# Performance work log

Hardware: AMD Instinct MI355X
Metric: run time of the kernel (lower is better)

The kernel has to match this reference:

```python
import jax, jax.numpy as jnp
from jax import lax
import numpy as np

ARG_NAMES = ('x w1 b1 bn1_g bn1_b bn1_m bn1_v w2 b2 bn2_g bn2_b bn2_m bn2_v w3 b3 w4 b4 '
             'attn_w attn_b attn_u g0_w1 g0_b1 g0_w2 g0_b2 g1_w1 g1_b1 g1_w2 g1_b2 '
             'g2_w1 g2_b1 g2_w2 g2_b2 c_w1 c_b1 c_w2 c_b2 c_w3 c_b3 c_w4 c_b4').split()


def _conv1d(x, w, b, stride, pad):
    # x: [N, C, L], w: [O, I, K]
    y = lax.conv_general_dilated(x, w, (stride,), [(pad, pad)],
                                 dimension_numbers=('NCH', 'OIH', 'NCH'))
    return y + b[None, :, None]


def _bn(x, g, b, m, v, eps=1e-5):
    # eval-mode BatchNorm1d over channel dim of [N, C, L]
    inv = g / jnp.sqrt(v + eps)
    return (x - m[None, :, None]) * inv[None, :, None] + b[None, :, None]


def _forward(x, w1, b1, bn1_g, bn1_b, bn1_m, bn1_v, w2, b2, bn2_g, bn2_b, bn2_m, bn2_v,
             w3, b3, w4, b4, attn_w, attn_b, attn_u,
             g0_w1, g0_b1, g0_w2, g0_b2, g1_w1, g1_b1, g1_w2, g1_b2,
             g2_w1, g2_b1, g2_w2, g2_b2,
             c_w1, c_b1, c_w2, c_b2, c_w3, c_b3, c_w4, c_b4):
    B, S, C, T = x.shape  # [batch, crops, channels=64, time=400]
    h = x.reshape(-1, C, T)
    # CNN stack (dropout = identity in eval)
    h = _bn(jax.nn.elu(_conv1d(h, w1, b1, 2, 1)), bn1_g, bn1_b, bn1_m, bn1_v)   # [N,64,192]
    h = _bn(jax.nn.elu(_conv1d(h, w2, b2, 2, 0)), bn2_g, bn2_b, bn2_m, bn2_v)   # [N,64,87]
    h = jax.nn.elu(_conv1d(h, w3, b3, 1, 0))                                    # [N,64,82]
    h = lax.reduce_window(h, 0.0, lax.add, (1, 1, 3), (1, 1, 2), 'VALID') / 3.0  # [N,64,40]
    h = jax.nn.elu(_conv1d(h, w4, b4, 1, 0))                                    # [N,64,35]
    h = h.reshape(B, S, C, -1)  # [B, S, 64, 35]
    # Attention pooling over the crop dim (dim=1), sum=True
    v = jnp.tanh(jnp.einsum('bsch,hd->bscd', h, attn_w) + attn_b)
    alphas = jax.nn.softmax(jnp.einsum('bscd,d->bsc', v, attn_u), axis=1)
    h = jax.nn.elu((h * alphas[..., None]).sum(axis=1))  # [B, 64, 35]
    # GIN over complete 64-node graph (self-loops included, eps=0):
    # aggregation per node == sum over all nodes of the graph
    def gin(h, W1, B1, W2, B2):
        agg = h + h.sum(axis=1, keepdims=True)
        return jax.nn.relu(agg @ W1 + B1) @ W2 + B2
    h = jax.nn.relu(gin(h, g0_w1, g0_b1, g0_w2, g0_b2))
    h = jax.nn.relu(gin(h, g1_w1, g1_b1, g1_w2, g1_b2))
    h = gin(h, g2_w1, g2_b1, g2_w2, g2_b2)  # no act after last layer
    # Classifier
    f = h.reshape(B, -1)  # [B, 2240]
    f = jax.nn.elu(f @ c_w1 + c_b1)
    f = jax.nn.elu(f @ c_w2 + c_b2)
    f = jax.nn.elu(f @ c_w3 + c_b3)
    return f @ c_w4 + c_b4  # [B, 2]


def setup_inputs() -> dict:
    key = jax.random.key(0)
    ks = iter(jax.random.split(key, 64))
    def rn(shape, s=0.05):
        return jax.random.normal(next(ks), shape, dtype=jnp.float32) * s
    d = {}
    d['x'] = jax.random.normal(next(ks), (32, 16, 64, 400), dtype=jnp.float32)
    d['w1'] = rn((64, 64, 20)); d['b1'] = rn((64,))
    d['bn1_g'] = jnp.ones((64,), jnp.float32); d['bn1_b'] = jnp.zeros((64,), jnp.float32)
    d['bn1_m'] = jnp.zeros((64,), jnp.float32); d['bn1_v'] = jnp.ones((64,), jnp.float32)
    d['w2'] = rn((64, 64, 20)); d['b2'] = rn((64,))
    d['bn2_g'] = jnp.ones((64,), jnp.float32); d['bn2_b'] = jnp.zeros((64,), jnp.float32)
    d['bn2_m'] = jnp.zeros((64,), jnp.float32); d['bn2_v'] = jnp.ones((64,), jnp.float32)
    d['w3'] = rn((64, 64, 6)); d['b3'] = rn((64,))
    d['w4'] = rn((64, 64, 6)); d['b4'] = rn((64,))
    d['attn_w'] = rn((35, 256), 0.1); d['attn_b'] = rn((256,), 0.1); d['attn_u'] = rn((256,), 0.1)
    d['g0_w1'] = rn((35, 256)); d['g0_b1'] = rn((256,))
    d['g0_w2'] = rn((256, 256)); d['g0_b2'] = rn((256,))
    d['g1_w1'] = rn((256, 256)); d['g1_b1'] = rn((256,))
    d['g1_w2'] = rn((256, 256)); d['g1_b2'] = rn((256,))
    d['g2_w1'] = rn((256, 35)); d['g2_b1'] = rn((35,))
    d['g2_w2'] = rn((35, 35)); d['g2_b2'] = rn((35,))
    d['c_w1'] = rn((2240, 256)); d['c_b1'] = rn((256,))
    d['c_w2'] = rn((256, 64)); d['c_b2'] = rn((64,))
    d['c_w3'] = rn((64, 16)); d['c_b3'] = rn((16,))
    d['c_w4'] = rn((16, 2)); d['c_b4'] = rn((2,))
    return d


def reference(x, w1, b1, bn1_g, bn1_b, bn1_m, bn1_v, w2, b2, bn2_g, bn2_b, bn2_m, bn2_v,
              w3, b3, w4, b4, attn_w, attn_b, attn_u,
              g0_w1, g0_b1, g0_w2, g0_b2, g1_w1, g1_b1, g1_w2, g1_b2,
              g2_w1, g2_b1, g2_w2, g2_b2,
              c_w1, c_b1, c_w2, c_b2, c_w3, c_b3, c_w4, c_b4):
    return _forward(x, w1, b1, bn1_g, bn1_b, bn1_m, bn1_v, w2, b2, bn2_g, bn2_b, bn2_m, bn2_v,
                    w3, b3, w4, b4, attn_w, attn_b, attn_u,
                    g0_w1, g0_b1, g0_w2, g0_b2, g1_w1, g1_b1, g1_w2, g1_b2,
                    g2_w1, g2_b1, g2_w2, g2_b2,
                    c_w1, c_b1, c_w2, c_b2, c_w3, c_b3, c_w4, c_b4)
```

## Files before the change

### kernel.cpp

```cpp
#include <hip/hip_runtime.h>
#include <math.h>

typedef __attribute__((ext_vector_type(8))) __bf16 bf16x8;
typedef __attribute__((ext_vector_type(4))) __bf16 bf16x4;
typedef __attribute__((ext_vector_type(4))) float f32x4;

__device__ __forceinline__ float elu_f(float v) {
    return v > 0.f ? v : (expf(v) - 1.f);
}

__global__ __launch_bounds__(256) void prep_weights(
    const float* __restrict__ w1, const float* __restrict__ w2,
    const float* __restrict__ w3, const float* __restrict__ w4,
    __bf16* __restrict__ t1, __bf16* __restrict__ t2,
    __bf16* __restrict__ t3, __bf16* __restrict__ t4)
{
    int idx = blockIdx.x * 256 + threadIdx.x;
    if (idx < 81920) {
        int k = idx / 4096, r = idx - k * 4096, co = r >> 6, ci = r & 63;
        t1[idx] = (__bf16)w1[(co * 64 + ci) * 20 + k];
    } else if (idx < 163840) {
        int j = idx - 81920;
        int k = j / 4096, r = j - k * 4096, co = r >> 6, ci = r & 63;
        t2[j] = (__bf16)w2[(co * 64 + ci) * 20 + k];
    } else if (idx < 188416) {
        int j = idx - 163840;
        int k = j / 4096, r = j - k * 4096, co = r >> 6, ci = r & 63;
        t3[j] = (__bf16)w3[(co * 64 + ci) * 6 + k];
    } else if (idx < 212992) {
        int j = idx - 188416;
        int k = j / 4096, r = j - k * 4096, co = r >> 6, ci = r & 63;
        t4[j] = (__bf16)w4[(co * 64 + ci) * 6 + k];
    }
}

__global__ __launch_bounds__(256) void prep_tr(
    const float* __restrict__ g0w1, const float* __restrict__ g0w2,
    const float* __restrict__ g1w1, const float* __restrict__ g1w2,
    const float* __restrict__ g2w1, const float* __restrict__ g2w2,
    __bf16* __restrict__ d0, __bf16* __restrict__ d1, __bf16* __restrict__ d2,
    __bf16* __restrict__ d3, __bf16* __restrict__ d4, __bf16* __restrict__ d5)
{
    int bid = blockIdx.x;
    const float* src; __bf16* dst; int K, O, Kpad, Opad, tile;
    if (bid < 4)       { src = g0w1; dst = d0; K = 35;   O = 256; Kpad = 64;   Opad = 256; tile = bid; }
    else if (bid < 20) { src = g0w2; dst = d1; K = 256;  O = 256; Kpad = 256;  Opad = 256; tile = bid - 4; }
    else if (bid < 36) { src = g1w1; dst = d2; K = 256;  O = 256; Kpad = 256;  Opad = 256; tile = bid - 20; }
    else if (bid < 52) { src = g1w2; dst = d3; K = 256;  O = 256; Kpad = 256;  Opad = 256; tile = bid - 36; }
    else if (bid < 56) { src = g2w1; dst = d4; K = 256;  O = 35;  Kpad = 256;  Opad = 64;  tile = bid - 52; }
    else               { src = g2w2; dst = d5; K = 35;   O = 35;  Kpad = 64;   Opad = 64;  tile = 0; }
    int ktiles = Kpad >> 6;
    int ot = tile / ktiles, kt = tile - ot * ktiles;
    int k0 = kt * 64, o0 = ot * 64;
    size_t LOFF = (size_t)Opad * Kpad;
    __shared__ float tl[64][68];
    int c = threadIdx.x & 63, rr = threadIdx.x >> 6;
    #pragma unroll
    for (int it = 0; it < 16; ++it) {
        int r = rr + it * 4;
        int kk = k0 + r, oo = o0 + c;
        tl[r][c] = (kk < K && oo < O) ? src[(size_t)kk * O + oo] : 0.f;
    }
    __syncthreads();
    #pragma unroll
    for (int it = 0; it < 16; ++it) {
        int r = rr + it * 4;
        float v = tl[c][r];
        __bf16 hi = (__bf16)v;
        float lo = v - (float)hi;
        size_t pos = (size_t)(o0 + r) * Kpad + k0 + c;
        dst[pos] = hi;
        dst[LOFF + pos] = (__bf16)lo;
    }
}

__global__ __launch_bounds__(256, 2) void conv1_mfma(
    const float* __restrict__ x, const __bf16* __restrict__ wT,
    const float* __restrict__ bias,
    const float* __restrict__ bn_g, const float* __restrict__ bn_b,
    const float* __restrict__ bn_m, const float* __restrict__ bn_v,
    __bf16* __restrict__ y)
{
    constexpr int LIN = 400, LOUT = 192, PAD = 1;
    constexpr int ROWS = 201;
    __shared__ __align__(16) __bf16 sx[2 * ROWS * 72];

    const int tid = threadIdx.x;
    const int n = blockIdx.x;
    const int wave = tid >> 6, lane = tid & 63;
    const int m = lane & 15, quad = lane >> 4;

    {
        const float* xg = x + (size_t)n * 64 * LIN;
        if (tid < 128) {
            int v = (tid >> 6) ? 401 : 0;
            sx[((v & 1) * ROWS + (v >> 1)) * 72 + (tid & 63)] = (__bf16)0.f;
        }
        constexpr int ITEMS = 16 * (LIN / 4);
        #pragma unroll
        for (int it = 0; it < 7; ++it) {
            int idx = it * 256 + tid;
            if (idx < ITEMS) {
                int jj = idx & 3;
                int g  = (idx >> 2) & 15;
                int q  = (idx >> 6) * 4 + jj;
                const float* xp = xg + (size_t)(4 * g) * LIN + 4 * q;
                float fa[4][4];
                #pragma unroll
                for (int u = 0; u < 4; ++u)
                    *(float4*)&fa[u][0] = *(const float4*)(xp + (size_t)u * LIN);
                #pragma unroll
                for (int e = 0; e < 4; ++e) {
                    int v = 4 * q + e + PAD;
                    bf16x4 wv = { (__bf16)fa[0][e], (__bf16)fa[1][e],
                                  (__bf16)fa[2][e], (__bf16)fa[3][e] };
                    *(bf16x4*)&sx[((v & 1) * ROWS + (v >> 1)) * 72 + 4 * g] = wv;
                }
            }
        }
    }

    const __bf16* wb = wT + (size_t)m * 64 + quad * 8;
    bf16x8 bb[2][2][4];
    #pragma unroll
    for (int p = 0; p < 2; ++p)
        #pragma unroll
        for (int s = 0; s < 2; ++s)
            #pragma unroll
            for (int nj = 0; nj < 4; ++nj)
                bb[p][s][nj] = *(const bf16x8*)(wb + (size_t)p * 4096 +
                                                nj * (16 * 64) + s * 32);

    __syncthreads();

    const int tile = wave;
    f32x4 acc[3][4];
    #pragma unroll
    for (int mi = 0; mi < 3; ++mi)
        #pragma unroll
        for (int nj = 0; nj < 4; ++nj)
            acc[mi][nj] = (f32x4){0.f, 0.f, 0.f, 0.f};

    #pragma unroll
    for (int kp = 0; kp < 20; ++kp) {
        const int buf = kp & 1, rowoff = kp >> 1;
        const __bf16* abase = sx + ((size_t)buf * ROWS + tile * 48 + m + rowoff) * 72;
        #pragma unroll
        for (int s = 0; s < 2; ++s) {
            bf16x8 af[3];
            #pragma unroll
            for (int mi = 0; mi < 3; ++mi)
                af[mi] = *(const bf16x8*)(abase + mi * (16 * 72) + s * 32 + quad * 8);
            #pragma unroll
            for (int mi = 0; mi < 3; ++mi)
                #pragma unroll
                for (int nj = 0; nj < 4; ++nj)
                    acc[mi][nj] = __builtin_amdgcn_mfma_f32_16x16x32_bf16(
                        af[mi], bb[kp & 1][s][nj], acc[mi][nj], 0, 0, 0);
        }
        if (kp + 2 < 20) {
            #pragma unroll
            for (int s = 0; s < 2; ++s)
                #pragma unroll
                for (int nj = 0; nj < 4; ++nj)
                    bb[kp & 1][s][nj] = *(const bf16x8*)(wb + (size_t)(kp + 2) * 4096 +
                                                         nj * (16 * 64) + s * 32);
        }
    }

    #pragma unroll
    for (int nj = 0; nj < 4; ++nj) {
        const int co = nj * 16 + m;
        const float bi = bias[co];
        const float inv   = bn_g[co] / sqrtf(bn_v[co] + 1e-5f);
        const float shift = bn_b[co] - bn_m[co] * inv;
        #pragma unroll
        for (int mi = 0; mi < 3; ++mi)
            #pragma unroll
            for (int r = 0; r < 4; ++r) {
                int t = tile * 48 + mi * 16 + quad * 4 + r;
                float v = elu_f(acc[mi][nj][r] + bi) * inv + shift;
                y[((size_t)n * LOUT + t) * 64 + co] = (__bf16)v;
            }
    }
}

__global__ __launch_bounds__(512, 2) void conv234_fused(
    const __bf16* __restrict__ h1,
    const __bf16* __restrict__ wT2, const float* __restrict__ b2,
    const float* __restrict__ bn2g, const float* __restrict__ bn2b,
    const float* __restrict__ bn2m, const float* __restrict__ bn2v,
    const __bf16* __restrict__ wT3, const float* __restrict__ b3,
    const __bf16* __restrict__ wT4, const float* __restrict__ b4,
    __bf16* __restrict__ h4)
{
    __shared__ __align__(16) __bf16 bufA[2 * 96 * 72];
    __shared__ __align__(16) __bf16 bufB[87 * 72];

    const int tid = threadIdx.x;
    const int n = blockIdx.x;
    const int wave = tid >> 6, lane = tid & 63;
    const int m = lane & 15, quad = lane >> 4;
    const int th  = wave >> 2;
    const int coq = wave & 3;

    {
        const __bf16* src = h1 + (size_t)n * 192 * 64;
        #pragma unroll
        for (int it = 0; it < 3; ++it) {
            int idx = it * 512 + tid;
            int v = idx >> 3, c8 = (idx & 7) * 8;
            *(uint4*)(bufA + ((size_t)(v & 1) * 96 + (v >> 1)) * 72 + c8) =
                *(const uint4*)(src + (size_t)v * 64 + c8);
        }
    }
    __syncthreads();

    {
        const __bf16* wb = wT2 + (size_t)(coq * 16 + m) * 64 + quad * 8;
        bf16x8 bw[20][2];
        #pragma unroll
        for (int kp = 0; kp < 20; ++kp)
            #pragma unroll
            for (int s = 0; s < 2; ++s)
                bw[kp][s] = *(const bf16x8*)(wb + (size_t)kp * 4096 + s * 32);

        f32x4 acc[3];
        #pragma unroll
        for (int mi = 0; mi < 3; ++mi) acc[mi] = (f32x4){0.f, 0.f, 0.f, 0.f};

        #pragma unroll
        for (int kp = 0; kp < 20; ++kp) {
            const int buf = kp & 1, rowoff = kp >> 1;
            const int r0 = th * 48 + m + rowoff;
            #pragma unroll
            for (int s = 0; s < 2; ++s) {
                bf16x8 af[3];
                #pragma unroll
                for (int mi = 0; mi < 3; ++mi) {
                    int rr = r0 + mi * 16; if (rr > 95) rr = 95;
                    af[mi] = *(const bf16x8*)(bufA + ((size_t)buf * 96 + rr) * 72 + s * 32 + quad * 8);
                }
                #pragma unroll
                for (int mi = 0; mi < 3; ++mi)
                    acc[mi] = __builtin_amdgcn_mfma_f32_16x16x32_bf16(
                        af[mi], bw[kp][s], acc[mi], 0, 0, 0);
            }
        }

        const int co = coq * 16 + m;
        const float bi = b2[co];
        float inv = bn2g[co] / sqrtf(bn2v[co] + 1e-5f);
        float shift = bn2b[co] - bn2m[co] * inv;
        #pragma unroll
        for (int mi = 0; mi < 3; ++mi)
            #pragma unroll
            for (int r = 0; r < 4; ++r) {
                int t = th * 48 + mi * 16 + quad * 4 + r;
                if (t < 87) {
                    float v = elu_f(acc[mi][r] + bi) * inv + shift;
                    bufB[t * 72 + co] = (__bf16)v;
                }
            }
    }
    __syncthreads();

    {
        const __bf16* wb = wT3 + (size_t)(coq * 16 + m) * 64 + quad * 8;
        bf16x8 bw[6][2];
        #pragma unroll
        for (int kp = 0; kp < 6; ++kp)
            #pragma unroll
            for (int s = 0; s < 2; ++s)
                bw[kp][s] = *(const bf16x8*)(wb + (size_t)kp * 4096 + s * 32);

        f32x4 acc[3];
        #pragma unroll
        for (int mi = 0; mi < 3; ++mi) acc[mi] = (f32x4){0.f, 0.f, 0.f, 0.f};

        #pragma unroll
        for (int kp = 0; kp < 6; ++kp) {
            const int r0 = th * 48 + m + kp;
            #pragma unroll
            for (int s = 0; s < 2; ++s) {
                bf16x8 af[3];
                #pragma unroll
                for (int mi = 0; mi < 3; ++mi) {
                    int rr = r0 + mi * 16; if (rr > 86) rr = 86;
                    af[mi] = *(const bf16x8*)(bufB + (size_t)rr * 72 + s * 32 + quad * 8);
                }
                #pragma unroll
                for (int mi = 0; mi < 3; ++mi)
                    acc[mi] = __builtin_amdgcn_mfma_f32_16x16x32_bf16(
                        af[mi], bw[kp][s], acc[mi], 0, 0, 0);
            }
        }

        const int co = coq * 16 + m;
        const float bi = b3[co];
        #pragma unroll
        for (int mi = 0; mi < 3; ++mi)
            #pragma unroll
            for (int r = 0; r < 4; ++r) {
                int t = th * 48 + mi * 16 + quad * 4 + r;
                if (t < 82)
                    bufA[t * 72 + co] = (__bf16)elu_f(acc[mi][r] + bi);
            }
    }
    __syncthreads();

    #pragma unroll
    for (int it = 0; it < 5; ++it) {
        int idx = it * 512 + tid;
        int t = idx >> 6, co = idx & 63;
        float v = ((float)bufA[(2 * t) * 72 + co] + (float)bufA[(2 * t + 1) * 72 + co] +
                   (float)bufA[(2 * t + 2) * 72 + co]) * (1.f / 3.f);
        bufB[t * 72 + co] = (__bf16)v;
    }
    __syncthreads();

    if (wave < 4) {
        const int co0 = wave * 16;
        const __bf16* wb = wT4 + (size_t)(co0 + m) * 64 + quad * 8;
        bf16x8 bw[6][2];
        #pragma unroll
        for (int kp = 0; kp < 6; ++kp)
            #pragma unroll
            for (int s = 0; s < 2; ++s)
                bw[kp][s] = *(const bf16x8*)(wb + (size_t)kp * 4096 + s * 32);

        f32x4 acc4[3];
        #pragma unroll
        for (int mi = 0; mi < 3; ++mi) acc4[mi] = (f32x4){0.f, 0.f, 0.f, 0.f};

        #pragma unroll
        for (int kp = 0; kp < 6; ++kp) {
            const int r0 = m + kp;
            #pragma unroll
            for (int s = 0; s < 2; ++s) {
                bf16x8 af[3];
                #pragma unroll
                for (int mi = 0; mi < 3; ++mi) {
                    int rr = r0 + mi * 16; if (rr > 39) rr = 39;
                    af[mi] = *(const bf16x8*)(bufB + (size_t)rr * 72 + s * 32 + quad * 8);
                }
                #pragma unroll
                for (int mi = 0; mi < 3; ++mi)
                    acc4[mi] = __builtin_amdgcn_mfma_f32_16x16x32_bf16(
                        af[mi], bw[kp][s], acc4[mi], 0, 0, 0);
            }
        }

        const int co = co0 + m;
        const float bi = b4[co];
        #pragma unroll
        for (int mi = 0; mi < 3; ++mi)
            #pragma unroll
            for (int r = 0; r < 4; ++r) {
                int t = mi * 16 + quad * 4 + r;
                if (t < 35)
                    h4[((size_t)n * 35 + t) * 64 + co] = (__bf16)elu_f(acc4[mi][r] + bi);
            }
    }
}

__global__ __launch_bounds__(256) void attn_pool_k(
    const __bf16* __restrict__ h, const float* __restrict__ W,
    const float* __restrict__ ab, const float* __restrict__ u,
    float* __restrict__ out)
{
    __shared__ float sW[35 * 256];
    __shared__ float sh[4][16 * 35 + 5];
    const int tid = threadIdx.x;
    const int pair0 = blockIdx.x * 4;
    for (int i = tid; i < 35 * 256; i += 256) sW[i] = W[i];
    for (int i = tid; i < 4 * 560; i += 256) {
        int q = i / 560, r = i - q * 560;
        int s = r / 35, t = r - s * 35;
        int bc = pair0 + q, b = bc >> 6, c = bc & 63;
        sh[q][s * 35 + t] = (float)h[(((size_t)b * 16 + s) * 35 + t) * 64 + c];
    }
    __syncthreads();

    const int wave = tid >> 6, lane = tid & 63;
    const int bc = pair0 + wave;
    const float* shw = sh[wave];

    float myu[4], myb[4];
    #pragma unroll
    for (int p = 0; p < 4; ++p) { myu[p] = u[lane + 64 * p]; myb[p] = ab[lane + 64 * p]; }

    float dot[16][4];
    #pragma unroll
    for (int s = 0; s < 16; ++s)
        #pragma unroll
        for (int p = 0; p < 4; ++p) dot[s][p] = myb[p];

    for (int t = 0; t < 35; ++t) {
        float w0 = sW[t * 256 + lane];
        float w1 = sW[t * 256 + lane + 64];
        float w2 = sW[t * 256 + lane + 128];
        float w3 = sW[t * 256 + lane + 192];
        #pragma unroll
        for (int s = 0; s < 16; ++s) {
            float hv = shw[s * 35 + t];
            dot[s][0] = fmaf(hv, w0, dot[s][0]);
            dot[s][1] = fmaf(hv, w1, dot[s][1]);
            dot[s][2] = fmaf(hv, w2, dot[s][2]);
            dot[s][3] = fmaf(hv, w3, dot[s][3]);
        }
    }

    float sc[16];
    #pragma unroll
    for (int s = 0; s < 16; ++s) {
        float v = tanhf(dot[s][0]) * myu[0] + tanhf(dot[s][1]) * myu[1]
                + tanhf(dot[s][2]) * myu[2] + tanhf(dot[s][3]) * myu[3];
        #pragma unroll
        for (int off = 1; off < 64; off <<= 1) v += __shfl_xor(v, off, 64);
        sc[s] = v;
    }

    float mx = sc[0];
    #pragma unroll
    for (int s = 1; s < 16; ++s) mx = fmaxf(mx, sc[s]);
    float e[16], sum = 0.f;
    #pragma unroll
    for (int s = 0; s < 16; ++s) { e[s] = expf(sc[s] - mx); sum += e[s]; }
    float inv = 1.f / sum;

    if (lane < 35) {
        float acc = 0.f;
        #pragma unroll
        for (int s = 0; s < 16; ++s) acc = fmaf(shw[s * 35 + lane], e[s] * inv, acc);
        out[(size_t)bc * 35 + lane] = elu_f(acc);
    }
}

#define APLANE (64 * 264)

__device__ __forceinline__ void gin_gemm_dev(
    const __bf16* As,
    const __bf16* __restrict__ Wg, int Kpad, int wlo, int Kout,
    const float* __restrict__ bias,
    int mode, __bf16* Ad, float* __restrict__ outg)
{
    const int lane = threadIdx.x & 63;
    const int wave = threadIdx.x >> 6;
    const int o0 = wave * 32;
    if (o0 >= ((Kout + 63) & ~63)) return;
    const int m = lane & 15, quad = lane >> 4;

    f32x4 acc[4][2];
    #pragma unroll
    for (int mi = 0; mi < 4; ++mi)
        #pragma unroll
        for (int nj = 0; nj < 2; ++nj)
            acc[mi][nj] = (f32x4){0.f, 0.f, 0.f, 0.f};

    for (int k0 = 0; k0 < Kpad; k0 += 32) {
        bf16x8 ah[4], al[4], bh[2], bl[2];
        #pragma unroll
        for (int mi = 0; mi < 4; ++mi) {
            const __bf16* ap = As + (size_t)(mi * 16 + m) * 264 + k0 + quad * 8;
            ah[mi] = *(const bf16x8*)ap;
            al[mi] = *(const bf16x8*)(ap + APLANE);
        }
        #pragma unroll
        for (int nj = 0; nj < 2; ++nj) {
            const __bf16* wp = Wg + (size_t)(o0 + nj * 16 + m) * Kpad + k0 + quad * 8;
            bh[nj] = *(const bf16x8*)wp;
            bl[nj] = *(const bf16x8*)(wp + wlo);
        }
        #pragma unroll
        for (int mi = 0; mi < 4; ++mi)
            #pragma unroll
            for (int nj = 0; nj < 2; ++nj) {
                acc[mi][nj] = __builtin_amdgcn_mfma_f32_16x16x32_bf16(
                    al[mi], bh[nj], acc[mi][nj], 0, 0, 0);
                acc[mi][nj] = __builtin_amdgcn_mfma_f32_16x16x32_bf16(
                    ah[mi], bl[nj], acc[mi][nj], 0, 0, 0);
                acc[mi][nj] = __builtin_amdgcn_mfma_f32_16x16x32_bf16(
                    ah[mi], bh[nj], acc[mi][nj], 0, 0, 0);
            }
    }

    #pragma unroll
    for (int nj = 0; nj < 2; ++nj) {
        const int o = o0 + nj * 16 + m;
        const bool ovalid = (o < Kout);
        const float bi = ovalid ? bias[o] : 0.f;
        float v[4][4];
        #pragma unroll
        for (int mi = 0; mi < 4; ++mi)
            #pragma unroll
            for (int r = 0; r < 4; ++r)
                v[mi][r] = acc[mi][nj][r] + bi;
        if (mode == 2) {
            if (ovalid) {
                #pragma unroll
                for (int mi = 0; mi < 4; ++mi)
                    #pragma unroll
                    for (int r = 0; r < 4; ++r)
                        outg[(size_t)(mi * 16 + quad * 4 + r) * Kout + o] = v[mi][r];
            }
        } else {
            float s = 0.f;
            #pragma unroll
            for (int mi = 0; mi < 4; ++mi)
                #pragma unroll
                for (int r = 0; r < 4; ++r) {
                    float rv = ovalid ? fmaxf(v[mi][r], 0.f) : 0.f;
                    v[mi][r] = rv;
                    s += rv;
                }
            if (mode == 1) {
                s += __shfl_xor(s, 16, 64);
                s += __shfl_xor(s, 32, 64);
            } else {
                s = 0.f;
            }
            #pragma unroll
            for (int mi = 0; mi < 4; ++mi)
                #pragma unroll
                for (int r = 0; r < 4; ++r) {
                    float a = v[mi][r] + s;
                    __bf16 hi = (__bf16)a;
                    size_t pos = (size_t)(mi * 16 + quad * 4 + r) * 264 + o;
                    Ad[pos] = hi;
                    Ad[APLANE + pos] = (__bf16)(a - (float)hi);
                }
        }
    }
}

__global__ __launch_bounds__(512) void gin_fused(
    const float* __restrict__ ha,
    const __bf16* __restrict__ gW0a, const __bf16* __restrict__ gW0b,
    const __bf16* __restrict__ gW1a, const __bf16* __restrict__ gW1b,
    const __bf16* __restrict__ gW2a, const __bf16* __restrict__ gW2b,
    const float* __restrict__ b0a, const float* __restrict__ b0b,
    const float* __restrict__ b1a, const float* __restrict__ b1b,
    const float* __restrict__ b2a, const float* __restrict__ b2b,
    float* __restrict__ H3)
{
    const int b = blockIdx.x, tid = threadIdx.x;
    __shared__ __align__(16) __bf16 sA[2][2 * APLANE];
    __shared__ float sS[64];
    const float* hab = ha + (size_t)b * 2240;

    if (tid < 64) {
        float s = 0.f;
        if (tid < 35)
            for (int n = 0; n < 64; ++n) s += hab[n * 35 + tid];
        sS[tid] = s;
    }
    __syncthreads();
    for (int idx = tid; idx < 64 * 64; idx += 512) {
        int n = idx >> 6, k = idx & 63;
        float a = (k < 35) ? hab[n * 35 + k] + sS[k] : 0.f;
        __bf16 hi = (__bf16)a;
        sA[0][n * 264 + k] = hi;
        sA[0][APLANE + n * 264 + k] = (__bf16)(a - (float)hi);
    }
    __syncthreads();

    gin_gemm_dev(sA[0], gW0a, 64,  16384, 256, b0a, 0, sA[1], nullptr); __syncthreads();
    gin_gemm_dev(sA[1], gW0b, 256, 65536, 256, b0b, 1, sA[0], nullptr); __syncthreads();
    gin_gemm_dev(sA[0], gW1a, 256, 65536, 256, b1a, 0, sA[1], nullptr); __syncthreads();
    gin_gemm_dev(sA[1], gW1b, 256, 65536, 256, b1b, 1, sA[0], nullptr); __syncthreads();
    gin_gemm_dev(sA[0], gW2a, 256, 16384, 35,  b2a, 0, sA[1], nullptr); __syncthreads();
    gin_gemm_dev(sA[1], gW2b, 64,  4096,  35,  b2b, 2, nullptr, H3 + (size_t)b * 2240);
}

__global__ __launch_bounds__(256) void cls1_part_k(
    const float* __restrict__ H3, const float* __restrict__ w1,
    float* __restrict__ s1p)
{
    const int b  = blockIdx.x;
    const int kc = blockIdx.y;
    const int k0 = kc * 140;
    __shared__ float sH[140];
    const int tid = threadIdx.x;
    if (tid < 140) sH[tid] = H3[(size_t)b * 2240 + k0 + tid];
    __syncthreads();
    const int o = (tid >> 6) * 64 + (tid & 63);
    float a0 = 0.f, a1 = 0.f, a2 = 0.f, a3 = 0.f;
    const float* wr = w1 + (size_t)k0 * 256 + o;
    #pragma unroll
    for (int k = 0; k < 140; k += 4) {
        a0 = fmaf(sH[k],     wr[(size_t)k * 256],       a0);
        a1 = fmaf(sH[k + 1], wr[(size_t)(k + 1) * 256], a1);
        a2 = fmaf(sH[k + 2], wr[(size_t)(k + 2) * 256], a2);
        a3 = fmaf(sH[k + 3], wr[(size_t)(k + 3) * 256], a3);
    }
    s1p[((size_t)kc * 32 + b) * 256 + o] = a0 + a1 + a2 + a3;
}

__global__ __launch_bounds__(256) void cls234_k(
    const float* __restrict__ s1p, const float* __restrict__ b1,
    const float* __restrict__ w2, const float* __restrict__ b2,
    const float* __restrict__ w3, const float* __restrict__ b3,
    const float* __restrict__ w4, const float* __restrict__ b4,
    float* __restrict__ out)
{
    const int b = blockIdx.x, tid = threadIdx.x;
    __shared__ float s1[256];
    __shared__ float part[4][64];
    __shared__ float s2[64];
    __shared__ float s3[16];
    {
        float acc = b1[tid];
        #pragma unroll
        for (int kc = 0; kc < 16; ++kc)
            acc += s1p[((size_t)kc * 32 + b) * 256 + tid];
        s1[tid] = elu_f(acc);
    }
    __syncthreads();
    {
        int kg = tid >> 6, o = tid & 63;
        float acc = 0.f;
        for (int k = kg * 64; k < kg * 64 + 64; ++k)
            acc = fmaf(s1[k], w2[k * 64 + o], acc);
        part[kg][o] = acc;
    }
    __syncthreads();
    if (tid < 64) {
        float acc = part[0][tid] + part[1][tid] + part[2][tid] + part[3][tid] + b2[tid];
        s2[tid] = elu_f(acc);
    }
    __syncthreads();
    if (tid < 16) {
        float acc = b3[tid];
        for (int k = 0; k < 64; ++k) acc = fmaf(s2[k], w3[k * 16 + tid], acc);
        s3[tid] = elu_f(acc);
    }
    __syncthreads();
    if (tid < 2) {
        float acc = b4[tid];
        for (int k = 0; k < 16; ++k) acc = fmaf(s3[k], w4[k * 2 + tid], acc);
        out[b * 2 + tid] = acc;
    }
}

extern "C" void kernel_launch(void* const* d_in, const int* in_sizes, int n_in,
                              void* d_out, int out_size, void* d_ws, size_t ws_size,
                              hipStream_t stream)
{
    const float* x     = (const float*)d_in[0];
    const float* w1    = (const float*)d_in[1];
    const float* b1    = (const float*)d_in[2];
    const float* bn1_g = (const float*)d_in[3];
    const float* bn1_b = (const float*)d_in[4];
    const float* bn1_m = (const float*)d_in[5];
    const float* bn1_v = (const float*)d_in[6];
    const float* w2    = (const float*)d_in[7];
    const float* b2    = (const float*)d_in[8];
    const float* bn2_g = (const float*)d_in[9];
    const float* bn2_b = (const float*)d_in[10];
    const float* bn2_m = (const float*)d_in[11];
    const float* bn2_v = (const float*)d_in[12];
    const float* w3    = (const float*)d_in[13];
    const float* b3    = (const float*)d_in[14];
    const float* w4    = (const float*)d_in[15];
    const float* b4    = (const float*)d_in[16];
    const float* attn_w = (const float*)d_in[17];
    const float* attn_b = (const float*)d_in[18];
    const float* attn_u = (const float*)d_in[19];
    const float* g0_w1 = (const float*)d_in[20];
    const float* g0_b1 = (const float*)d_in[21];
    const float* g0_w2 = (const float*)d_in[22];
    const float* g0_b2 = (const float*)d_in[23];
    const float* g1_w1 = (const float*)d_in[24];
    const float* g1_b1 = (const float*)d_in[25];
    const float* g1_w2 = (const float*)d_in[26];
    const float* g1_b2 = (const float*)d_in[27];
    const float* g2_w1 = (const float*)d_in[28];
    const float* g2_b1 = (const float*)d_in[29];
    const float* g2_w2 = (const float*)d_in[30];
    const float* g2_b2 = (const float*)d_in[31];
    const float* c_w1  = (const float*)d_in[32];
    const float* c_b1  = (const float*)d_in[33];
    const float* c_w2  = (const float*)d_in[34];
    const float* c_b2  = (const float*)d_in[35];
    const float* c_w3  = (const float*)d_in[36];
    const float* c_b3  = (const float*)d_in[37];
    const float* c_w4  = (const float*)d_in[38];
    const float* c_b4  = (const float*)d_in[39];
    float* out = (float*)d_out;

    char* ws = (char*)d_ws;
    __bf16* wT1  = (__bf16*)(ws + 0);
    __bf16* wT2  = (__bf16*)(ws + 163840);
    __bf16* wT3  = (__bf16*)(ws + 327680);
    __bf16* wT4  = (__bf16*)(ws + 376832);
    __bf16* h1   = (__bf16*)(ws + 425984);
    __bf16* h4   = (__bf16*)(ws + 13008896);
    float*  ha   = (float*)(ws + 15302656);
    __bf16* gW0a = (__bf16*)(ws + 15589376);
    __bf16* gW0b = (__bf16*)(ws + 15654912);
    __bf16* gW1a = (__bf16*)(ws + 15917056);
    __bf16* gW1b = (__bf16*)(ws + 16179200);
    __bf16* gW2a = (__bf16*)(ws + 16441344);
    __bf16* gW2b = (__bf16*)(ws + 16506880);
    float*  H3   = (float*)(ws + 16523264);
    float*  s1p  = (float*)(ws + 16809984);

    prep_weights<<<dim3(832), dim3(256), 0, stream>>>(w1, w2, w3, w4, wT1, wT2, wT3, wT4);
    prep_tr<<<dim3(57), dim3(256), 0, stream>>>(g0_w1, g0_w2, g1_w1, g1_w2, g2_w1, g2_w2,
                                                gW0a, gW0b, gW1a, gW1b, gW2a, gW2b);

    conv1_mfma<<<dim3(512), dim3(256), 0, stream>>>(
        x, wT1, b1, bn1_g, bn1_b, bn1_m, bn1_v, h1);

    conv234_fused<<<dim3(512), dim3(512), 0, stream>>>(
        h1, wT2, b2, bn2_g, bn2_b, bn2_m, bn2_v, wT3, b3, wT4, b4, h4);

    attn_pool_k<<<dim3(512), dim3(256), 0, stream>>>(h4, attn_w, attn_b, attn_u, ha);

    gin_fused<<<dim3(32), dim3(512), 0, stream>>>(
        ha, gW0a, gW0b, gW1a, gW1b, gW2a, gW2b,
        g0_b1, g0_b2, g1_b1, g1_b2, g2_b1, g2_b2, H3);

    cls1_part_k<<<dim3(32, 16), dim3(256), 0, stream>>>(H3, c_w1, s1p);
    cls234_k<<<dim3(32), dim3(256), 0, stream>>>(s1p, c_b1, c_w2, c_b2, c_w3, c_b3,
                                                 c_w4, c_b4, out);
}
```

Baseline: 317.4 us.

## Split conv1 output channels across twice the waves and stage weights in LDS

```diff
diff --git a/kernel.cpp b/kernel.cpp
--- a/kernel.cpp
+++ b/kernel.cpp
@@ -74,7 +74,7 @@
     }
 }
 
-__global__ __launch_bounds__(256, 2) void conv1_mfma(
+__global__ __launch_bounds__(512, 2) void conv1_mfma(
     const float* __restrict__ x, const __bf16* __restrict__ wT,
     const float* __restrict__ bias,
     const float* __restrict__ bn_g, const float* __restrict__ bn_b,
@@ -84,11 +84,14 @@
     constexpr int LIN = 400, LOUT = 192, PAD = 1;
     constexpr int ROWS = 201;
     __shared__ __align__(16) __bf16 sx[2 * ROWS * 72];
+    __shared__ __align__(16) __bf16 sw[2 * 64 * 72];
 
     const int tid = threadIdx.x;
     const int n = blockIdx.x;
     const int wave = tid >> 6, lane = tid & 63;
     const int m = lane & 15, quad = lane >> 4;
+    const int tile = wave >> 1;
+    const int coh  = (wave & 1) * 32;
 
     {
         const float* xg = x + (size_t)n * 64 * LIN;
@@ -98,8 +101,8 @@
         }
         constexpr int ITEMS = 16 * (LIN / 4);
         #pragma unroll
-        for (int it = 0; it < 7; ++it) {
-            int idx = it * 256 + tid;
+        for (int it = 0; it < 4; ++it) {
+            int idx = it * 512 + tid;
             if (idx < ITEMS) {
                 int jj = idx & 3;
                 int g  = (idx >> 2) & 15;
@@ -120,57 +123,52 @@
         }
     }
 
-    const __bf16* wb = wT + (size_t)m * 64 + quad * 8;
-    bf16x8 bb[2][2][4];
-    #pragma unroll
-    for (int p = 0; p < 2; ++p)
-        #pragma unroll
-        for (int s = 0; s < 2; ++s)
-            #pragma unroll
-            for (int nj = 0; nj < 4; ++nj)
-                bb[p][s][nj] = *(const bf16x8*)(wb + (size_t)p * 4096 +
-                                                nj * (16 * 64) + s * 32);
-
-    __syncthreads();
-
-    const int tile = wave;
-    f32x4 acc[3][4];
+    f32x4 acc[3][2];
     #pragma unroll
     for (int mi = 0; mi < 3; ++mi)
         #pragma unroll
-        for (int nj = 0; nj < 4; ++nj)
+        for (int nj = 0; nj < 2; ++nj)
             acc[mi][nj] = (f32x4){0.f, 0.f, 0.f, 0.f};
 
-    #pragma unroll
-    for (int kp = 0; kp < 20; ++kp) {
-        const int buf = kp & 1, rowoff = kp >> 1;
-        const __bf16* abase = sx + ((size_t)buf * ROWS + tile * 48 + m + rowoff) * 72;
-        #pragma unroll
-        for (int s = 0; s < 2; ++s) {
-            bf16x8 af[3];
-            #pragma unroll
-            for (int mi = 0; mi < 3; ++mi)
-                af[mi] = *(const bf16x8*)(abase + mi * (16 * 72) + s * 32 + quad * 8);
-            #pragma unroll
-            for (int mi = 0; mi < 3; ++mi)
-                #pragma unroll
-                for (int nj = 0; nj < 4; ++nj)
-                    acc[mi][nj] = __builtin_amdgcn_mfma_f32_16x16x32_bf16(
-                        af[mi], bb[kp & 1][s][nj], acc[mi][nj], 0, 0, 0);
-        }
-        if (kp + 2 < 20) {
-            #pragma unroll
-            for (int s = 0; s < 2; ++s)
-                #pragma unroll
-                for (int nj = 0; nj < 4; ++nj)
-                    bb[kp & 1][s][nj] = *(const bf16x8*)(wb + (size_t)(kp + 2) * 4096 +
-                                                         nj * (16 * 64) + s * 32);
-        }
-    }
-
-    #pragma unroll
-    for (int nj = 0; nj < 4; ++nj) {
-        const int co = nj * 16 + m;
+    for (int kb = 0; kb < 20; kb += 2) {
+        if (kb) __syncthreads();
+        #pragma unroll
+        for (int i = 0; i < 2; ++i) {
+            int idx = i * 512 + tid;
+            int r = idx >> 3, p = idx & 7;
+            *(uint4*)(sw + (size_t)r * 72 + p * 8) =
+                *(const uint4*)(wT + (size_t)(kb + (r >> 6)) * 4096 + (r & 63) * 64 + p * 8);
+        }
+        __syncthreads();
+
+        #pragma unroll
+        for (int kp2 = 0; kp2 < 2; ++kp2) {
+            const int kp = kb + kp2;
+            const int buf = kp & 1, rowoff = kp >> 1;
+            const __bf16* abase = sx + ((size_t)buf * ROWS + tile * 48 + m + rowoff) * 72;
+            const __bf16* bbase = sw + (size_t)(kp2 * 64 + coh + m) * 72;
+            #pragma unroll
+            for (int s = 0; s < 2; ++s) {
+                bf16x8 af[3], bfr[2];
+                #pragma unroll
+                for (int mi = 0; mi < 3; ++mi)
+                    af[mi] = *(const bf16x8*)(abase + mi * (16 * 72) + s * 32 + quad * 8);
+                #pragma unroll
+                for (int nj = 0; nj < 2; ++nj)
+                    bfr[nj] = *(const bf16x8*)(bbase + nj * (16 * 72) + s * 32 + quad * 8);
+                #pragma unroll
+                for (int mi = 0; mi < 3; ++mi)
+                    #pragma unroll
+                    for (int nj = 0; nj < 2; ++nj)
+                        acc[mi][nj] = __builtin_amdgcn_mfma_f32_16x16x32_bf16(
+                            af[mi], bfr[nj], acc[mi][nj], 0, 0, 0);
+            }
+        }
+    }
+
+    #pragma unroll
+    for (int nj = 0; nj < 2; ++nj) {
+        const int co = coh + nj * 16 + m;
         const float bi = bias[co];
         const float inv   = bn_g[co] / sqrtf(bn_v[co] + 1e-5f);
         const float shift = bn_b[co] - bn_m[co] * inv;
@@ -710,7 +708,7 @@
     prep_tr<<<dim3(57), dim3(256), 0, stream>>>(g0_w1, g0_w2, g1_w1, g1_w2, g2_w1, g2_w2,
                                                 gW0a, gW0b, gW1a, gW1b, gW2a, gW2b);
 
-    conv1_mfma<<<dim3(512), dim3(256), 0, stream>>>(
+    conv1_mfma<<<dim3(512), dim3(512), 0, stream>>>(
         x, wT1, b1, bn1_g, bn1_b, bn1_m, bn1_v, h1);
 
     conv234_fused<<<dim3(512), dim3(512), 0, stream>>>(
```

New measurement: 298.6 us. 1.06x faster.
